# Kernel tuning notes

Hardware: AMD Instinct MI355X
Metric: run time of the kernel (lower is better)

The kernel has to match this reference:

```python
import jax, jax.numpy as jnp
import numpy as np

D = 2  # spatial dimension


def conv_contract(x, filt, k_in, k_out):
    """Equivariant convolve-then-contract for one (in,out) type pair.
    x: (B, Cin, H, W) + (D,)*k_in
    filt: (O, Cin, 3, 3) + (D,)*k_in + (D,)*k_out
    The first k_in tensor indices of the filter contract with the image's
    tensor indices (absorbed into the conv's input-feature dimension).
    Torus (periodic) padding, stride 1, as per padding='TORUS'.
    """
    B, Cin, H, W = x.shape[0], x.shape[1], x.shape[2], x.shape[3]
    O = filt.shape[0]
    din, dout = D ** k_in, D ** k_out
    # fold tensor-in components into input channels: (B, Cin*din, H, W)
    xr = jnp.moveaxis(x.reshape(B, Cin, H, W, din), -1, 2).reshape(B, Cin * din, H, W)
    # filter -> (O*dout, Cin*din, 3, 3) with matching (Cin, din) ordering
    fr = filt.reshape(O, Cin, 3, 3, din, dout)
    fr = jnp.transpose(fr, (0, 5, 1, 4, 2, 3)).reshape(O * dout, Cin * din, 3, 3)
    # periodic padding then VALID conv == TORUS padding
    xp = jnp.pad(xr, ((0, 0), (0, 0), (1, 1), (1, 1)), mode='wrap')
    out = jax.lax.conv_general_dilated(xp, fr, (1, 1), 'VALID',
                                       dimension_numbers=('NCHW', 'OIHW', 'NCHW'))
    out = jnp.moveaxis(out.reshape(B, O, dout, H, W), 2, -1)  # (B,O,H,W,dout)
    return out.reshape((B, O, H, W) + (D,) * k_out)


def setup_inputs() -> dict:
    key = jax.random.key(0)
    ks = jax.random.split(key, 11)
    B, Cin, Cout, H, W = 8, 96, 96, 128, 128
    N0, N1, N2 = 3, 4, 5  # num invariant filters for tensor order 0,1,2
    b0 = 1.0 / np.sqrt(Cin * 9)
    b1 = 1.0 / np.sqrt(Cin * 9 * D)
    inp = {
        'x_scalar': jax.random.normal(ks[0], (B, Cin, H, W), dtype=jnp.float32),
        'x_vector': jax.random.normal(ks[1], (B, Cin, H, W, D), dtype=jnp.float32),
        'f_k0': jax.random.normal(ks[2], (N0, 3, 3), dtype=jnp.float32),
        'f_k1': jax.random.normal(ks[3], (N1, 3, 3, D), dtype=jnp.float32),
        'f_k2': jax.random.normal(ks[4], (N2, 3, 3, D, D), dtype=jnp.float32),
        'w_ss': jax.random.uniform(ks[5], (Cout, Cin, N0), minval=-b0, maxval=b0),
        'w_sv': jax.random.uniform(ks[6], (Cout, Cin, N1), minval=-b0, maxval=b0),
        'w_vs': jax.random.uniform(ks[7], (Cout, Cin, N1), minval=-b1, maxval=b1),
        'w_vv': jax.random.uniform(ks[8], (Cout, Cin, N2), minval=-b1, maxval=b1),
        'b_s': jax.random.uniform(ks[9], (Cout, 1, 1), minval=-b0, maxval=b0),
        'b_v': jax.random.uniform(ks[10], (Cout, 1, 1, 1), minval=-b1, maxval=b1),
    }
    return inp


def reference(x_scalar, x_vector, f_k0, f_k1, f_k2, w_ss, w_sv, w_vs, w_vv, b_s, b_v):
    # build per-pair filters: weights (O,I,N) x invariant filters (N, 3,3, D^k...)
    f_k0 = jax.lax.stop_gradient(f_k0)
    f_k1 = jax.lax.stop_gradient(f_k1)
    f_k2 = jax.lax.stop_gradient(f_k2)
    F_ss = jnp.einsum('oin,nhw->oihw', w_ss, f_k0)        # scalar->scalar
    F_sv = jnp.einsum('oin,nhwa->oihwa', w_sv, f_k1)      # scalar->vector
    F_vs = jnp.einsum('oin,nhwa->oihwa', w_vs, f_k1)      # vector->scalar
    F_vv = jnp.einsum('oin,nhwab->oihwab', w_vv, f_k2)    # vector->vector
    # convolve each input type against each output type, contract in-tensor
    # indices, and sum contributions per output type
    out_s = conv_contract(x_scalar, F_ss, 0, 0) + conv_contract(x_vector, F_vs, 1, 0)
    out_v = conv_contract(x_scalar, F_sv, 0, 1) + conv_contract(x_vector, F_vv, 1, 1)
    # use_bias='auto': regular bias for scalars, mean-scaled bias for non-scalars
    out_s = out_s + b_s[None]
    out_v = out_v + b_v[None] * jnp.mean(out_v, axis=(2, 3), keepdims=True)
    return out_s, out_v
```

## Files before the change

kernel.cpp:

```cpp
#include <hip/hip_runtime.h>

#define HWSZ 16384
#define CIN 96
#define ICTOT 288
#define OUT_S_ELEMS (8*96*16384)
#define TILE_USH (ICTOT*32)
#define NTILES 81

typedef __attribute__((ext_vector_type(8))) short bf16x8;
typedef __attribute__((ext_vector_type(4))) float f32x4;

#define VMCNT(n) asm volatile("s_waitcnt vmcnt(" #n ")" ::: "memory")

__device__ __forceinline__ unsigned short f2bf(float f){
  unsigned int u = __float_as_uint(f);
  u += 0x7FFFu + ((u >> 16) & 1u);
  return (unsigned short)(u >> 16);
}

__device__ __forceinline__ void gload16(const unsigned short* g, const unsigned short* l){
  __builtin_amdgcn_global_load_lds(
      (const __attribute__((address_space(1))) unsigned int*)g,
      (__attribute__((address_space(3))) unsigned int*)l, 16, 0, 0);
}

__global__ void pack_w_kernel(const float* __restrict__ w_ss, const float* __restrict__ w_sv,
                              const float* __restrict__ w_vs, const float* __restrict__ w_vv,
                              const float* __restrict__ f_k0, const float* __restrict__ f_k1,
                              const float* __restrict__ f_k2, unsigned short* __restrict__ WbT){
  int idx = blockIdx.x*256 + threadIdx.x;
  if (idx >= NTILES*ICTOT*32) return;
  int j = idx / (ICTOT*32); int rem = idx - j*(ICTOT*32);
  int oc = rem >> 5, cc = rem & 31;
  int tap = j % 9, cch = j / 9;
  int ic = cch*32 + cc;
  float acc = 0.f;
  if (oc < 96){
    int o = oc;
    if (ic < CIN){
      int i = ic;
      for (int n=0;n<3;++n) acc += w_ss[(o*CIN+i)*3+n]*f_k0[n*9+tap];
    } else {
      int v = ic-CIN; int i=v>>1, a=v&1;
      for (int n=0;n<4;++n) acc += w_vs[(o*CIN+i)*4+n]*f_k1[(n*9+tap)*2+a];
    }
  } else {
    int ov = oc-96; int o=ov>>1, c=ov&1;
    if (ic < CIN){
      int i = ic;
      for (int n=0;n<4;++n) acc += w_sv[(o*CIN+i)*4+n]*f_k1[(n*9+tap)*2+c];
    } else {
      int v = ic-CIN; int i=v>>1, a=v&1;
      for (int n=0;n<5;++n) acc += w_vv[(o*CIN+i)*5+n]*f_k2[((n*9+tap)*2+a)*2+c];
    }
  }
  WbT[(size_t)j*TILE_USH + oc*32 + cc] = f2bf(acc);
}

__global__ void pack_x_kernel(const float* __restrict__ xs, const float* __restrict__ xv,
                              unsigned short* __restrict__ Xp, float* __restrict__ Part){
  __shared__ float2 tile[32][65];
  __shared__ float red[2][8][32];
  int bid0 = blockIdx.x;
  int t = threadIdx.x;
  if (bid0 < 6144){
    int bid = bid0;
    int ct = bid % 3; int pt = (bid/3) & 255; int b = bid / 768;
    int p0 = pt*64, c0 = ct*32;
    float* tf = (float*)tile;
    int cl = t >> 6, pl = t & 63;
    for (int kk=0; kk<8; ++kk){
      int c = kk*4 + cl;
      tf[c*130 + pl] = xs[(size_t)(b*CIN + c0 + c)*HWSZ + p0 + pl];
    }
    __syncthreads();
    int c = t & 31, pw = t >> 5;
    float psum = 0.f;
    for (int j=0;j<8;++j){
      int p = pw*8 + j;
      float v = tf[c*130 + p];
      psum += v;
      Xp[(size_t)(b*HWSZ + p0 + p)*ICTOT + c0 + c] = f2bf(v);
    }
    red[0][pw][c] = psum;
    __syncthreads();
    if (t < 32){
      float s = 0.f;
      #pragma unroll
      for (int k=0;k<8;++k) s += red[0][k][t];
      Part[((size_t)b*ICTOT + c0 + t)*256 + pt] = s;
    }
  } else {
    int bid = bid0 - 6144;
    int ct = bid % 3; int pt = (bid/3) & 255; int b = bid / 768;
    int p0 = pt*64, c0 = ct*32;
    int cl = t >> 6, pl = t & 63;
    const float2* src = (const float2*)xv;
    for (int kk=0; kk<8; ++kk){
      int c = kk*4 + cl;
      tile[c][pl] = src[(size_t)(b*CIN + c0 + c)*HWSZ + p0 + pl];
    }
    __syncthreads();
    int c = t & 31, pw = t >> 5;
    float sx = 0.f, sy = 0.f;
    for (int j=0;j<8;++j){
      int p = pw*8 + j;
      float2 v = tile[c][p];
      sx += v.x; sy += v.y;
      unsigned int u = (unsigned int)f2bf(v.x) | ((unsigned int)f2bf(v.y) << 16);
      *(unsigned int*)&Xp[(size_t)(b*HWSZ + p0 + p)*ICTOT + CIN + 2*(c0+c)] = u;
    }
    red[0][pw][c] = sx; red[1][pw][c] = sy;
    __syncthreads();
    if (t < 32){
      float s0 = 0.f, s1 = 0.f;
      #pragma unroll
      for (int k=0;k<8;++k){ s0 += red[0][k][t]; s1 += red[1][k][t]; }
      Part[((size_t)b*ICTOT + CIN + 2*(c0+t)    )*256 + pt] = s0;
      Part[((size_t)b*ICTOT + CIN + 2*(c0+t) + 1)*256 + pt] = s1;
    }
  }
}

__global__ void reduce_part_kernel(const float* __restrict__ Part, float* __restrict__ Ssum){
  int b = blockIdx.x;
  int t = threadIdx.x;
  if (t >= ICTOT) return;
  const float* p = Part + ((size_t)b*ICTOT + t)*256;
  float s = 0.f;
  #pragma unroll 8
  for (int i=0;i<256;++i) s += p[i];
  Ssum[b*ICTOT + t] = s;
}

__global__ void mbias_kernel(const float* __restrict__ w_sv, const float* __restrict__ w_vv,
                             const float* __restrict__ f_k1, const float* __restrict__ f_k2,
                             const float* __restrict__ b_v, const float* __restrict__ Ssum,
                             float* __restrict__ MB){
  int row = blockIdx.x;
  int o = row >> 1, c = row & 1;
  int lane = threadIdx.x;
  float f1s[4], f2s[5][2];
  for (int n=0;n<4;++n){
    float s=0.f;
    for (int tap=0;tap<9;++tap) s += f_k1[(n*9+tap)*2+c];
    f1s[n]=s;
  }
  for (int n=0;n<5;++n)
    for (int a=0;a<2;++a){
      float s=0.f;
      for (int tap=0;tap<9;++tap) s += f_k2[((n*9+tap)*2+a)*2+c];
      f2s[n][a]=s;
    }
  float wv[5];
  for (int k=0;k<5;++k){
    int ic = lane + 64*k;
    float v = 0.f;
    if (ic < CIN){
      for (int n=0;n<4;++n) v += w_sv[(o*CIN+ic)*4+n]*f1s[n];
    } else if (ic < ICTOT){
      int u = ic-CIN; int i=u>>1, a=u&1;
      for (int n=0;n<5;++n) v += w_vv[(o*CIN+i)*5+n]*f2s[n][a];
    }
    wv[k] = v;
  }
  for (int b=0;b<8;++b){
    float acc = 0.f;
    for (int k=0;k<5;++k){
      int ic = lane + 64*k;
      if (ic < ICTOT) acc += wv[k]*Ssum[b*ICTOT+ic];
    }
    for (int m=1;m<64;m<<=1) acc += __shfl_xor(acc, m);
    if (lane == 0) MB[b*192+row] = b_v[o]*acc*(1.f/16384.f);
  }
}

template<bool LASTC>
__device__ __forceinline__ void chunkG(int c, const char* WbTb,
    const unsigned short* Bcur, unsigned short* Bnxt,
    const unsigned short* const (&srcB)[4],
    int tid, int w, int jr0, int Aoffb, const int (&boff)[12],
    bf16x8 (&afc)[9], bf16x8 (&bfr)[4], f32x4 (&acc)[9][4])
{
  const int wl = w*512;
  const char* cbase = WbTb + (size_t)(9*c)*18432;
  #pragma unroll
  for (int t=0;t<9;++t){
    if (!LASTC && t==0){
      #pragma unroll
      for (int i=0;i<4;++i) gload16(srcB[i] + (c+1)*32, Bnxt + i*4096 + wl);
    }
    const char* cA1 = cbase + (size_t)(t+1)*18432;
    __builtin_amdgcn_s_setprio(1);
    #pragma unroll
    for (int m=0;m<9;++m){
      #pragma unroll
      for (int n=0;n<4;++n)
        acc[m][n] = __builtin_amdgcn_mfma_f32_16x16x32_bf16(afc[m], bfr[n], acc[m][n], 0,0,0);
      if (!(LASTC && t==8))
        afc[m] = *(const bf16x8*)(cA1 + Aoffb + m*1024);
    }
    __builtin_amdgcn_s_setprio(0);
    if (t < 8){
      const int tau = t+1, ky = tau/3, kx = tau%3;
      const unsigned short* Bj = Bcur + (jr0+ky)*4096;
      #pragma unroll
      for (int n=0;n<4;++n) bfr[n] = *(const bf16x8*)&Bj[boff[kx*4+n]];
    } else if (!LASTC){
      VMCNT(0);
      __builtin_amdgcn_s_barrier();
      __builtin_amdgcn_sched_barrier(0);
      const unsigned short* Bj = (const unsigned short*)Bnxt + jr0*4096;
      #pragma unroll
      for (int n=0;n<4;++n) bfr[n] = *(const bf16x8*)&Bj[boff[n]];
    }
  }
}

__global__ __launch_bounds__(512,2) void conv_mfma_kernel(
    const unsigned short* __restrict__ Xp, const unsigned short* __restrict__ WbT,
    const float* __restrict__ b_s, const float* __restrict__ MB,
    float* __restrict__ out){
  __shared__ unsigned short Bsh[2][16384];

  int bid = blockIdx.x;
  int b = bid & 7, rp = bid >> 3;
  int tid = threadIdx.x;
  int lane = tid & 63, w = tid >> 6;
  int wr = w >> 2, wc = w & 3;
  int cl = lane & 15, g = lane >> 4;

  f32x4 acc[9][4];
  #pragma unroll
  for (int m=0;m<9;++m)
    #pragma unroll
    for (int n=0;n<4;++n) acc[m][n] = (f32x4){0.f,0.f,0.f,0.f};

  const size_t xb = (size_t)b * HWSZ * ICTOT;
  const unsigned short* srcB[4];
  #pragma unroll
  for (int i=0;i<4;++i){
    int f = i*512 + tid;
    int j = f >> 9, px = (f >> 2) & 127, cp = f & 3;
    int cps = cp ^ ((px >> 1) & 3);
    int hs = (2*rp - 1 + j + 128) & 127;
    srcB[i] = Xp + xb + ((size_t)(hs*128 + px))*ICTOT + cps*8;
  }
  const int Aoffb = ((wr*144 + cl)*32 + g*8)*2;
  const int pxb = (wc & 1)*64 + cl;
  const int jr0 = (wc >> 1);

  int boff[12];
  #pragma unroll
  for (int kx=0;kx<3;++kx)
    #pragma unroll
    for (int n=0;n<4;++n){
      int px = (pxb + n*16 + kx + 127) & 127;
      boff[kx*4+n] = px*32 + ((g ^ ((px >> 1) & 3))*8);
    }

  const char* WbTb = (const char*)WbT;
  const int wl = w*512;

  #pragma unroll
  for (int i=0;i<4;++i) gload16(srcB[i], &Bsh[0][i*4096 + wl]);
  VMCNT(0);
  __builtin_amdgcn_s_barrier();
  __builtin_amdgcn_sched_barrier(0);

  bf16x8 afc[9], bfr[4];
  #pragma unroll
  for (int n=0;n<4;++n) bfr[n] = *(const bf16x8*)&Bsh[0][jr0*4096 + boff[n]];
  #pragma unroll
  for (int m=0;m<9;++m) afc[m] = *(const bf16x8*)(WbTb + Aoffb + m*1024);

  for (int c=0;c<8;++c){
    chunkG<false>(c, WbTb, &Bsh[c&1][0], &Bsh[(c&1)^1][0],
                  srcB, tid, w, jr0, Aoffb, boff, afc, bfr, acc);
  }
  chunkG<true>(8, WbTb, &Bsh[0][0], &Bsh[1][0],
               srcB, tid, w, jr0, Aoffb, boff, afc, bfr, acc);

  const int orow = 2*rp + (wc >> 1);
  const int colb = (wc & 1)*64;
  #pragma unroll
  for (int m=0;m<9;++m){
    int ocb = wr*144 + m*16 + 4*g;
    if (wr == 0 && m < 6){
      #pragma unroll
      for (int r=0;r<4;++r){
        int oc = ocb + r;
        float bias = b_s[oc];
        #pragma unroll
        for (int n=0;n<4;++n){
          int p = orow*128 + colb + n*16 + cl;
          out[(size_t)(b*96+oc)*HWSZ + p] = acc[m][n][r] + bias;
        }
      }
    } else {
      float2* outv = (float2*)(out + OUT_S_ELEMS);
      int row0 = ocb - 96;
      int o0 = row0 >> 1;
      float mb0 = MB[b*192+row0  ], mb1 = MB[b*192+row0+1];
      float mb2 = MB[b*192+row0+2], mb3 = MB[b*192+row0+3];
      #pragma unroll
      for (int n=0;n<4;++n){
        int p = orow*128 + colb + n*16 + cl;
        outv[(size_t)(b*96+o0  )*HWSZ + p] = (float2){acc[m][n][0]+mb0, acc[m][n][1]+mb1};
        outv[(size_t)(b*96+o0+1)*HWSZ + p] = (float2){acc[m][n][2]+mb2, acc[m][n][3]+mb3};
      }
    }
  }
}

extern "C" void kernel_launch(void* const* d_in, const int* in_sizes, int n_in,
                              void* d_out, int out_size, void* d_ws, size_t ws_size,
                              hipStream_t stream){
  const float* xs   = (const float*)d_in[0];
  const float* xv   = (const float*)d_in[1];
  const float* f_k0 = (const float*)d_in[2];
  const float* f_k1 = (const float*)d_in[3];
  const float* f_k2 = (const float*)d_in[4];
  const float* w_ss = (const float*)d_in[5];
  const float* w_sv = (const float*)d_in[6];
  const float* w_vs = (const float*)d_in[7];
  const float* w_vv = (const float*)d_in[8];
  const float* b_s  = (const float*)d_in[9];
  const float* b_v  = (const float*)d_in[10];
  float* out = (float*)d_out;

  char* ws = (char*)d_ws;
  unsigned short* WbT = (unsigned short*)ws;
  const size_t XP_OFF = (size_t)NTILES*TILE_USH*2 + 6144;
  unsigned short* Xp = (unsigned short*)(ws + XP_OFF);
  const size_t PART_OFF = XP_OFF + (size_t)8*HWSZ*ICTOT*2;
  float* Part = (float*)(ws + PART_OFF);
  float* Ssum = (float*)(ws + PART_OFF + 2359296);
  float* MB   = (float*)(ws + PART_OFF + 2359296 + 9216);

  pack_w_kernel<<<(NTILES*ICTOT*32 + 255)/256, 256, 0, stream>>>(
      w_ss, w_sv, w_vs, w_vv, f_k0, f_k1, f_k2, WbT);
  pack_x_kernel<<<12288, 256, 0, stream>>>(xs, xv, Xp, Part);
  reduce_part_kernel<<<8, 320, 0, stream>>>(Part, Ssum);
  mbias_kernel<<<192, 64, 0, stream>>>(w_sv, w_vv, f_k1, f_k2, b_v, Ssum, MB);
  conv_mfma_kernel<<<512, 512, 0, stream>>>(Xp, WbT, b_s, MB, out);
}
```

Measured before the change: 287.3 us.

## Stage weight slices through LDS triple buffer and split output channels across blocks

The conv kernel now uses 256-thread blocks, each covering half of the 288 output channels, so the grid doubles. Weight tiles are streamed into a swizzled triple-buffered LDS region with async global-to-LDS loads, replacing direct per-lane global loads into registers. The input tile buffer is single-buffered and refilled at the end of each channel chunk. This removes global-load latency from the weight path but doubles input-tile traffic and adds a barrier per tap.

```diff
diff --git a/kernel.cpp b/kernel.cpp
--- a/kernel.cpp
+++ b/kernel.cpp
@@ -5,12 +5,14 @@
 #define ICTOT 288
 #define OUT_S_ELEMS (8*96*16384)
 #define TILE_USH (ICTOT*32)
+#define ASLICE 4608
 #define NTILES 81
 
 typedef __attribute__((ext_vector_type(8))) short bf16x8;
 typedef __attribute__((ext_vector_type(4))) float f32x4;
 
 #define VMCNT(n) asm volatile("s_waitcnt vmcnt(" #n ")" ::: "memory")
+#define LGKM0    asm volatile("s_waitcnt lgkmcnt(0)" ::: "memory")
 
 __device__ __forceinline__ unsigned short f2bf(float f){
   unsigned int u = __float_as_uint(f);
@@ -54,7 +56,8 @@
       for (int n=0;n<5;++n) acc += w_vv[(o*CIN+i)*5+n]*f_k2[((n*9+tap)*2+a)*2+c];
     }
   }
-  WbT[(size_t)j*TILE_USH + oc*32 + cc] = f2bf(acc);
+  int cc_sw = ((((cc>>3) ^ ((oc>>1)&3)) << 3) | (cc & 7));
+  WbT[(size_t)j*TILE_USH + oc*32 + cc_sw] = f2bf(acc);
 }
 
 __global__ void pack_x_kernel(const float* __restrict__ xs, const float* __restrict__ xv,
@@ -176,59 +179,76 @@
 }
 
 template<bool LASTC>
-__device__ __forceinline__ void chunkG(int c, const char* WbTb,
-    const unsigned short* Bcur, unsigned short* Bnxt,
-    const unsigned short* const (&srcB)[4],
-    int tid, int w, int jr0, int Aoffb, const int (&boff)[12],
+__device__ __forceinline__ void chunk4(int c,
+    const unsigned short* __restrict__ WbT, int mt,
+    unsigned short (&Ash)[3][ASLICE], unsigned short* Bsh,
+    const unsigned short* P0, const unsigned short* P1, const int (&hsrow)[4],
+    int tid, int w, int jr0, int Abase, const int (&boff)[12],
     bf16x8 (&afc)[9], bf16x8 (&bfr)[4], f32x4 (&acc)[9][4])
 {
   const int wl = w*512;
-  const char* cbase = WbTb + (size_t)(9*c)*18432;
+  const unsigned short* srcA = WbT + (size_t)(9*c)*TILE_USH + mt*ASLICE + tid*8;
   #pragma unroll
   for (int t=0;t<9;++t){
-    if (!LASTC && t==0){
-      #pragma unroll
-      for (int i=0;i<4;++i) gload16(srcB[i] + (c+1)*32, Bnxt + i*4096 + wl);
-    }
-    const char* cA1 = cbase + (size_t)(t+1)*18432;
+    VMCNT(0);
+    if (!LASTC || t<=6){
+      const unsigned short* s = srcA + (size_t)(t+2)*TILE_USH;
+      unsigned short* d = Ash[(t+2)%3];
+      gload16(s,        d + wl);
+      gload16(s + 2048, d + 2048 + wl);
+      if (tid < 64) gload16(s + 4096, d + 4096);
+    }
+    if (!LASTC && t==8){
+      #pragma unroll
+      for (int i=0;i<8;++i){
+        const unsigned short* sB = ((i&1) ? P1 : P0) + hsrow[i>>1] + (c+1)*32;
+        gload16(sB, Bsh + i*2048 + wl);
+      }
+    }
+    const unsigned short* An = Ash[(t+1)%3];
     __builtin_amdgcn_s_setprio(1);
     #pragma unroll
     for (int m=0;m<9;++m){
       #pragma unroll
       for (int n=0;n<4;++n)
         acc[m][n] = __builtin_amdgcn_mfma_f32_16x16x32_bf16(afc[m], bfr[n], acc[m][n], 0,0,0);
-      if (!(LASTC && t==8))
-        afc[m] = *(const bf16x8*)(cA1 + Aoffb + m*1024);
+      if (!(LASTC && t==8)) afc[m] = *(const bf16x8*)&An[Abase + m*512];
     }
     __builtin_amdgcn_s_setprio(0);
     if (t < 8){
       const int tau = t+1, ky = tau/3, kx = tau%3;
-      const unsigned short* Bj = Bcur + (jr0+ky)*4096;
+      const unsigned short* Bj = Bsh + (jr0+ky)*4096;
       #pragma unroll
       for (int n=0;n<4;++n) bfr[n] = *(const bf16x8*)&Bj[boff[kx*4+n]];
+      if (t == 7) { LGKM0; }
+      __builtin_amdgcn_s_barrier();
     } else if (!LASTC){
       VMCNT(0);
       __builtin_amdgcn_s_barrier();
-      __builtin_amdgcn_sched_barrier(0);
-      const unsigned short* Bj = (const unsigned short*)Bnxt + jr0*4096;
+      const unsigned short* Bj = Bsh + jr0*4096;
       #pragma unroll
       for (int n=0;n<4;++n) bfr[n] = *(const bf16x8*)&Bj[boff[n]];
-    }
-  }
-}
-
-__global__ __launch_bounds__(512,2) void conv_mfma_kernel(
+      __builtin_amdgcn_s_barrier();
+    }
+  }
+}
+
+__global__ __launch_bounds__(256,2) void conv_mfma_kernel(
     const unsigned short* __restrict__ Xp, const unsigned short* __restrict__ WbT,
     const float* __restrict__ b_s, const float* __restrict__ MB,
     float* __restrict__ out){
-  __shared__ unsigned short Bsh[2][16384];
+  __shared__ unsigned short Ash[3][ASLICE];
+  __shared__ unsigned short Bsh[16384];
 
   int bid = blockIdx.x;
-  int b = bid & 7, rp = bid >> 3;
+  int b = bid & 7;
+  int rest = bid >> 3;
+  int mt = rest & 1, rp = rest >> 1;
   int tid = threadIdx.x;
   int lane = tid & 63, w = tid >> 6;
-  int wr = w >> 2, wc = w & 3;
   int cl = lane & 15, g = lane >> 4;
+  int jr0 = w >> 1;
+  const int pxb = (w & 1)*64 + cl;
 
   f32x4 acc[9][4];
   #pragma unroll
@@ -237,19 +257,15 @@
     for (int n=0;n<4;++n) acc[m][n] = (f32x4){0.f,0.f,0.f,0.f};
 
   const size_t xb = (size_t)b * HWSZ * ICTOT;
-  const unsigned short* srcB[4];
-  #pragma unroll
-  for (int i=0;i<4;++i){
-    int f = i*512 + tid;
-    int j = f >> 9, px = (f >> 2) & 127, cp = f & 3;
-    int cps = cp ^ ((px >> 1) & 3);
-    int hs = (2*rp - 1 + j + 128) & 127;
-    srcB[i] = Xp + xb + ((size_t)(hs*128 + px))*ICTOT + cps*8;
-  }
-  const int Aoffb = ((wr*144 + cl)*32 + g*8)*2;
-  const int pxb = (wc & 1)*64 + cl;
-  const int jr0 = (wc >> 1);
-
+  int q = tid >> 2;
+  int cps = (tid & 3) ^ ((tid >> 3) & 3);
+  const unsigned short* P0 = Xp + xb + (size_t)q*ICTOT + cps*8;
+  const unsigned short* P1 = P0 + 64*ICTOT;
+  int hsrow[4];
+  #pragma unroll
+  for (int j=0;j<4;++j) hsrow[j] = ((2*rp - 1 + j + 128) & 127) * 128 * ICTOT;
+
+  const int Abase = cl*32 + ((g ^ ((cl>>1)&3))*8);
   int boff[12];
   #pragma unroll
   for (int kx=0;kx<3;++kx)
@@ -259,34 +275,42 @@
       boff[kx*4+n] = px*32 + ((g ^ ((px >> 1) & 3))*8);
     }
 
-  const char* WbTb = (const char*)WbT;
   const int wl = w*512;
-
-  #pragma unroll
-  for (int i=0;i<4;++i) gload16(srcB[i], &Bsh[0][i*4096 + wl]);
+  #pragma unroll
+  for (int i=0;i<8;++i){
+    const unsigned short* sB = ((i&1) ? P1 : P0) + hsrow[i>>1];
+    gload16(sB, Bsh + i*2048 + wl);
+  }
+  const unsigned short* srcA0 = WbT + mt*ASLICE + tid*8;
+  #pragma unroll
+  for (int j=0;j<2;++j){
+    const unsigned short* s = srcA0 + (size_t)j*TILE_USH;
+    unsigned short* d = Ash[j];
+    gload16(s,        d + wl);
+    gload16(s + 2048, d + 2048 + wl);
+    if (tid < 64) gload16(s + 4096, d + 4096);
+  }
   VMCNT(0);
   __builtin_amdgcn_s_barrier();
-  __builtin_amdgcn_sched_barrier(0);
 
   bf16x8 afc[9], bfr[4];
   #pragma unroll
-  for (int n=0;n<4;++n) bfr[n] = *(const bf16x8*)&Bsh[0][jr0*4096 + boff[n]];
-  #pragma unroll
-  for (int m=0;m<9;++m) afc[m] = *(const bf16x8*)(WbTb + Aoffb + m*1024);
-
-  for (int c=0;c<8;++c){
-    chunkG<false>(c, WbTb, &Bsh[c&1][0], &Bsh[(c&1)^1][0],
-                  srcB, tid, w, jr0, Aoffb, boff, afc, bfr, acc);
-  }
-  chunkG<true>(8, WbTb, &Bsh[0][0], &Bsh[1][0],
-               srcB, tid, w, jr0, Aoffb, boff, afc, bfr, acc);
-
-  const int orow = 2*rp + (wc >> 1);
-  const int colb = (wc & 1)*64;
+  for (int n=0;n<4;++n) bfr[n] = *(const bf16x8*)&Bsh[jr0*4096 + boff[n]];
+  #pragma unroll
+  for (int m=0;m<9;++m) afc[m] = *(const bf16x8*)&Ash[0][Abase + m*512];
+
+  for (int c=0;c<8;++c)
+    chunk4<false>(c, WbT, mt, Ash, Bsh, P0, P1, hsrow,
+                  tid, w, jr0, Abase, boff, afc, bfr, acc);
+  chunk4<true>(8, WbT, mt, Ash, Bsh, P0, P1, hsrow,
+               tid, w, jr0, Abase, boff, afc, bfr, acc);
+
+  const int orow = 2*rp + jr0;
+  const int colb = (w & 1)*64;
   #pragma unroll
   for (int m=0;m<9;++m){
-    int ocb = wr*144 + m*16 + 4*g;
-    if (wr == 0 && m < 6){
+    int ocb = mt*144 + m*16 + 4*g;
+    if (mt == 0 && m < 6){
       #pragma unroll
       for (int r=0;r<4;++r){
         int oc = ocb + r;
@@ -343,5 +367,5 @@
   pack_x_kernel<<<12288, 256, 0, stream>>>(xs, xv, Xp, Part);
   reduce_part_kernel<<<8, 320, 0, stream>>>(Part, Ssum);
   mbias_kernel<<<192, 64, 0, stream>>>(w_sv, w_vv, f_k1, f_k2, b_v, Ssum, MB);
-  conv_mfma_kernel<<<512, 512, 0, stream>>>(Xp, WbT, b_s, MB, out);
-}
+  conv_mfma_kernel<<<1024, 256, 0, stream>>>(Xp, WbT, b_s, MB, out);
+}
```

Measured after the change: 267.0 us. 1.08x faster.
